# Kernel optimization log

Hardware: AMD Instinct MI355X
Metric: run time of the kernel (lower is better)

The kernel has to match this reference:

```python
import jax, jax.numpy as jnp
import numpy as np

B, D, H = 131072, 8, 128


def setup_inputs() -> dict:
    key = jax.random.key(0)
    ks = jax.random.split(key, 8)
    s1 = 1.0 / np.sqrt(D + 1)
    s2 = 1.0 / np.sqrt(H)
    return {
        "z": jax.random.normal(ks[0], (B, D), dtype=jnp.float32),
        "logp_z": jnp.zeros((B, 1), dtype=jnp.float32),
        "t": jax.random.uniform(ks[1], (1,), dtype=jnp.float32),
        "W1": jax.random.normal(ks[2], (D + 1, H), dtype=jnp.float32) * s1,
        "b1": jnp.zeros((H,), dtype=jnp.float32),
        "W2": jax.random.normal(ks[3], (H, H), dtype=jnp.float32) * s2,
        "b2": jnp.zeros((H,), dtype=jnp.float32),
        "W3": jax.random.normal(ks[4], (H, D), dtype=jnp.float32) * s2,
        "b3": jnp.zeros((D,), dtype=jnp.float32),
    }


def _net_single(z_i, t_scalar, W1, b1, W2, b2, W3, b3):
    # z_i: [D] -> dz/dt: [D]; FFJORD-style MLP on concat([z, t])
    x = jnp.concatenate([z_i, t_scalar[None]])  # [D+1]
    h = jnp.tanh(x @ W1 + b1)
    h = jnp.tanh(h @ W2 + b2)
    return h @ W3 + b3


def reference(z, logp_z, t, W1, b1, W2, b2, W3, b3):
    t_scalar = t.reshape(())

    def f_i(z_i):
        return _net_single(z_i, t_scalar, W1, b1, W2, b2, W3, b3)

    # dz/dt for every sample (batched forward)
    dz_dt = jax.vmap(f_i)(z)  # [B, D]
    # Exact Jacobian trace: fused forward-mode batched Jacobian (replaces the
    # original's D sequential autograd.grad reverse-mode calls)
    jac = jax.vmap(jax.jacfwd(f_i))(z)  # [B, D, D]
    trace = jnp.einsum("bii->b", jac)  # [B]
    dlogp_z_dt = -trace[:, None]  # [B, 1]
    return (dz_dt, dlogp_z_dt)
```

## Files before the change

### kernel.cpp

```cpp
#include <hip/hip_runtime.h>
#include <hip/hip_bf16.h>

#define BATCH 131072
#define PITCH_Q 40

typedef __bf16 bf16x8 __attribute__((ext_vector_type(8)));
typedef float floatx4 __attribute__((ext_vector_type(4)));

__device__ __forceinline__ float fast_tanh(float x) {
    float e = __expf(2.0f * x);
    return 1.0f - 2.0f * __builtin_amdgcn_rcpf(e + 1.0f);
}


__global__ void prep_kernel(const float* __restrict__ W1,
                            const float* __restrict__ W2,
                            const float* __restrict__ W3,
                            __bf16* __restrict__ ws) {
    int idx = blockIdx.x * 256 + threadIdx.x;
    if (idx < 16384) {
        int j = idx & 7, q = (idx >> 3) & 3, n = (idx >> 5) & 127, kb = idx >> 12;
        int k = kb * 32 + q * 8 + j;
        ws[idx] = (__bf16)W2[k * 128 + n];
        float c = 0.0f;
        #pragma unroll
        for (int d = 0; d < 8; ++d) c += W3[k * 8 + d] * W1[d * 128 + n];
        ws[16384 + idx] = (__bf16)(W2[n * 128 + k] * c);
    } else if (idx < 20480) {
        int t = idx - 16384;
        int j = t & 7, q = (t >> 3) & 3, n = t >> 5;
        int k = q * 8 + j;
        ws[32768 + t] = (k < 9) ? (__bf16)W1[k * 128 + n] : (__bf16)0.0f;
    } else if (idx < 22528) {
        int t = idx - 20480;
        int j = t & 7, q = (t >> 3) & 3, n = (t >> 5) & 15, kb = t >> 9;
        int k = kb * 32 + q * 8 + j;
        ws[36864 + t] = (n < 8) ? (__bf16)W3[k * 8 + n] : (__bf16)0.0f;
    }
}

__global__ __launch_bounds__(256, 2) void cnf_main(
        const float* __restrict__ z, const float* __restrict__ t_ptr,
        const float* __restrict__ b1g, const float* __restrict__ b2g,
        const float* __restrict__ b3g, const __bf16* __restrict__ ws,
        float* __restrict__ out) {
    __shared__ __bf16 sW2s[16384];
    __shared__ __bf16 sGTs[16384];
    __shared__ __align__(16) __bf16 tile[4][2][16 * PITCH_Q];

    const int tid = threadIdx.x;
    const int lane = tid & 63;
    const int w = tid >> 6;
    const int p = lane & 15;
    const int q = lane >> 4;
    const int sbase = blockIdx.x * 128 + w * 32;
    const float tval = t_ptr[0];

    bf16x8 ax0, ax1;
    #pragma unroll
    for (int j = 0; j < 8; ++j) { ax0[j] = (__bf16)0.0f; ax1[j] = (__bf16)0.0f; }
    if (q == 0) {
        const float4* zp0 = (const float4*)(z + (size_t)(sbase + p) * 8);
        const float4* zp1 = (const float4*)(z + (size_t)(sbase + 16 + p) * 8);
        const float4 a0 = zp0[0], a1 = zp0[1], c0 = zp1[0], c1 = zp1[1];
        ax0[0] = (__bf16)a0.x; ax0[1] = (__bf16)a0.y;
        ax0[2] = (__bf16)a0.z; ax0[3] = (__bf16)a0.w;
        ax0[4] = (__bf16)a1.x; ax0[5] = (__bf16)a1.y;
        ax0[6] = (__bf16)a1.z; ax0[7] = (__bf16)a1.w;
        ax1[0] = (__bf16)c0.x; ax1[1] = (__bf16)c0.y;
        ax1[2] = (__bf16)c0.z; ax1[3] = (__bf16)c0.w;
        ax1[4] = (__bf16)c1.x; ax1[5] = (__bf16)c1.y;
        ax1[6] = (__bf16)c1.z; ax1[7] = (__bf16)c1.w;
    } else if (q == 1) {
        ax0[0] = (__bf16)tval;
        ax1[0] = (__bf16)tval;
    }

    const bf16x8* W1g = (const bf16x8*)(ws + 32768);
    const bf16x8* W3g = (const bf16x8*)(ws + 36864);
    bf16x8 w1f[8];
    #pragma unroll
    for (int nt = 0; nt < 8; ++nt) w1f[nt] = W1g[(nt * 16 + p) * 4 + q];
    bf16x8 w3f[4];
    #pragma unroll
    for (int kb = 0; kb < 4; ++kb) w3f[kb] = W3g[(kb * 16 + p) * 4 + q];
    float b1f[8], b2f[8];
    #pragma unroll
    for (int nt = 0; nt < 8; ++nt) { b1f[nt] = b1g[nt * 16 + p]; b2f[nt] = b2g[nt * 16 + p]; }
    const float b3v = (p < 8) ? b3g[p] : 0.0f;

    {
        uint4* dst = (uint4*)sW2s;
        const uint4* src = (const uint4*)ws;
        #pragma unroll
        for (int i = 0; i < 8; ++i) dst[tid + i * 256] = src[tid + i * 256];
        uint4* dstg = (uint4*)sGTs;
        const uint4* srcg = (const uint4*)(ws + 16384);
        #pragma unroll
        for (int i = 0; i < 8; ++i) dstg[tid + i * 256] = srcg[tid + i * 256];
    }

    __bf16* Ta = tile[w][0];
    __bf16* Tb = tile[w][1];

    float a1c0[32], a1c1[32];
    bf16x8 ah0[4], ah1[4];
    #pragma unroll
    for (int c = 0; c < 4; ++c) {
        floatx4 aA[2], aB[2];
        #pragma unroll
        for (int lt = 0; lt < 2; ++lt) {
            floatx4 zz = {0.f, 0.f, 0.f, 0.f};
            aA[lt] = __builtin_amdgcn_mfma_f32_16x16x32_bf16(ax0, w1f[2 * c + lt], zz, 0, 0, 0);
            aB[lt] = __builtin_amdgcn_mfma_f32_16x16x32_bf16(ax1, w1f[2 * c + lt], zz, 0, 0, 0);
        }
        #pragma unroll
        for (int lt = 0; lt < 2; ++lt) {
            const int nt = 2 * c + lt;
            const float bn = b1f[nt];
            #pragma unroll
            for (int r = 0; r < 4; ++r) {
                const float h1a = fast_tanh(aA[lt][r] + bn);
                a1c0[nt * 4 + r] = __builtin_fmaf(-h1a, h1a, 1.0f);
                Ta[(q * 4 + r) * PITCH_Q + lt * 16 + p] = (__bf16)h1a;
                const float h1b = fast_tanh(aB[lt][r] + bn);
                a1c1[nt * 4 + r] = __builtin_fmaf(-h1b, h1b, 1.0f);
                Tb[(q * 4 + r) * PITCH_Q + lt * 16 + p] = (__bf16)h1b;
            }
        }
        ah0[c] = *(const bf16x8*)&Ta[p * PITCH_Q + q * 8];
        ah1[c] = *(const bf16x8*)&Tb[p * PITCH_Q + q * 8];
    }

    __syncthreads();
    const bf16x8* W2sv = (const bf16x8*)sW2s;
    const bf16x8* GTsv = (const bf16x8*)sGTs;

    bf16x8 ah2_0[4], ah2_1[4];
    #pragma unroll
    for (int c = 0; c < 4; ++c) {
        floatx4 aA[2] = {{0.f, 0.f, 0.f, 0.f}, {0.f, 0.f, 0.f, 0.f}};
        floatx4 aB[2] = {{0.f, 0.f, 0.f, 0.f}, {0.f, 0.f, 0.f, 0.f}};
        #pragma unroll
        for (int kb = 0; kb < 4; ++kb) {
            #pragma unroll
            for (int lt = 0; lt < 2; ++lt) {
                const int n = (2 * c + lt) * 16 + p;
                const bf16x8 wf = W2sv[(kb * 128 + n) * 4 + q];
                aA[lt] = __builtin_amdgcn_mfma_f32_16x16x32_bf16(ah0[kb], wf, aA[lt], 0, 0, 0);
                aB[lt] = __builtin_amdgcn_mfma_f32_16x16x32_bf16(ah1[kb], wf, aB[lt], 0, 0, 0);
            }
        }
        #pragma unroll
        for (int lt = 0; lt < 2; ++lt) {
            const int nt = 2 * c + lt;
            const float bn = b2f[nt];
            #pragma unroll
            for (int r = 0; r < 4; ++r) {
                const float h2a = fast_tanh(aA[lt][r] + bn);
                Ta[(q * 4 + r) * PITCH_Q + lt * 16 + p] = (__bf16)h2a;
                const float h2b = fast_tanh(aB[lt][r] + bn);
                Tb[(q * 4 + r) * PITCH_Q + lt * 16 + p] = (__bf16)h2b;
            }
        }
        ah2_0[c] = *(const bf16x8*)&Ta[p * PITCH_Q + q * 8];
        ah2_1[c] = *(const bf16x8*)&Tb[p * PITCH_Q + q * 8];
    }

    floatx4 d3A = {0.f, 0.f, 0.f, 0.f}, d3B = {0.f, 0.f, 0.f, 0.f};
    #pragma unroll
    for (int kb = 0; kb < 4; ++kb) {
        d3A = __builtin_amdgcn_mfma_f32_16x16x32_bf16(ah2_0[kb], w3f[kb], d3A, 0, 0, 0);
        d3B = __builtin_amdgcn_mfma_f32_16x16x32_bf16(ah2_1[kb], w3f[kb], d3B, 0, 0, 0);
    }
    if (p < 8) {
        #pragma unroll
        for (int r = 0; r < 4; ++r) {
            out[(size_t)(sbase + q * 4 + r) * 8 + p] = d3A[r] + b3v;
            out[(size_t)(sbase + 16 + q * 4 + r) * 8 + p] = d3B[r] + b3v;
        }
    }

    bf16x8 aa0[4], aa1[4];
    #pragma unroll
    for (int kb = 0; kb < 4; ++kb) {
        #pragma unroll
        for (int j = 0; j < 8; ++j) {
            const float fa = (float)ah2_0[kb][j];
            aa0[kb][j] = (__bf16)__builtin_fmaf(-fa, fa, 1.0f);
            const float fb = (float)ah2_1[kb][j];
            aa1[kb][j] = (__bf16)__builtin_fmaf(-fb, fb, 1.0f);
        }
    }

    float trA[4] = {0.f, 0.f, 0.f, 0.f}, trB[4] = {0.f, 0.f, 0.f, 0.f};
    #pragma unroll
    for (int nt = 0; nt < 8; ++nt) {
        const int n = nt * 16 + p;
        floatx4 uA = {0.f, 0.f, 0.f, 0.f}, uB = {0.f, 0.f, 0.f, 0.f};
        #pragma unroll
        for (int kb = 0; kb < 4; ++kb) {
            const bf16x8 gf = GTsv[(kb * 128 + n) * 4 + q];
            uA = __builtin_amdgcn_mfma_f32_16x16x32_bf16(aa0[kb], gf, uA, 0, 0, 0);
            uB = __builtin_amdgcn_mfma_f32_16x16x32_bf16(aa1[kb], gf, uB, 0, 0, 0);
        }
        #pragma unroll
        for (int r = 0; r < 4; ++r) {
            trA[r] = __builtin_fmaf(a1c0[nt * 4 + r], uA[r], trA[r]);
            trB[r] = __builtin_fmaf(a1c1[nt * 4 + r], uB[r], trB[r]);
        }
    }

    #pragma unroll
    for (int r = 0; r < 4; ++r) {
        float va = trA[r];
        va += __shfl_xor(va, 1, 64);
        va += __shfl_xor(va, 2, 64);
        va += __shfl_xor(va, 4, 64);
        va += __shfl_xor(va, 8, 64);
        trA[r] = va;
        float vb = trB[r];
        vb += __shfl_xor(vb, 1, 64);
        vb += __shfl_xor(vb, 2, 64);
        vb += __shfl_xor(vb, 4, 64);
        vb += __shfl_xor(vb, 8, 64);
        trB[r] = vb;
    }
    if (p == 0) {
        #pragma unroll
        for (int r = 0; r < 4; ++r) {
            out[(size_t)BATCH * 8 + sbase + q * 4 + r] = -trA[r];
            out[(size_t)BATCH * 8 + sbase + 16 + q * 4 + r] = -trB[r];
        }
    }
}

extern "C" void kernel_launch(void* const* d_in, const int* in_sizes, int n_in,
                              void* d_out, int out_size, void* d_ws, size_t ws_size,
                              hipStream_t stream) {
    const float* z  = (const float*)d_in[0];
    const float* t  = (const float*)d_in[2];
    const float* W1 = (const float*)d_in[3];
    const float* b1 = (const float*)d_in[4];
    const float* W2 = (const float*)d_in[5];
    const float* b2 = (const float*)d_in[6];
    const float* W3 = (const float*)d_in[7];
    const float* b3 = (const float*)d_in[8];
    __bf16* ws = (__bf16*)d_ws;
    float* out = (float*)d_out;

    prep_kernel<<<88, 256, 0, stream>>>(W1, W2, W3, ws);
    cnf_main<<<1024, 256, 0, stream>>>(z, t, b1, b2, b3, ws, out);
}
```

Baseline: 94.35 us.

## Transpose MFMA operand order, fold biases into accumulators and W1 padding

Swaps the A/B operands of every MFMA so outputs come out transposed (samples along lanes). Activations can then be written to the LDS tile as packed 4-element vectors, and outputs and traces stored with vector writes. The trace reduction becomes two cross-lane shuffles instead of four per row. b1 is folded into the padded K rows of W1 as a bf16 hi/lo split, b2 and b3 seed the accumulators, and the per-lane bias registers are dropped. The two per-wave tiles are merged into one wider tile. This cuts VALU work, LDS stores and register pressure, at the cost of slight precision changes in the bias handling.

```diff
diff --git a/kernel.cpp b/kernel.cpp
--- a/kernel.cpp
+++ b/kernel.cpp
@@ -2,8 +2,9 @@
 #include <hip/hip_bf16.h>
 
 #define BATCH 131072
-#define PITCH_Q 40
-
+#define PITCH_H 72
+
+typedef __bf16 bf16x4 __attribute__((ext_vector_type(4)));
 typedef __bf16 bf16x8 __attribute__((ext_vector_type(8)));
 typedef float floatx4 __attribute__((ext_vector_type(4)));
 
@@ -16,6 +17,7 @@
 __global__ void prep_kernel(const float* __restrict__ W1,
                             const float* __restrict__ W2,
                             const float* __restrict__ W3,
+                            const float* __restrict__ b1,
                             __bf16* __restrict__ ws) {
     int idx = blockIdx.x * 256 + threadIdx.x;
     if (idx < 16384) {
@@ -30,7 +32,14 @@
         int t = idx - 16384;
         int j = t & 7, q = (t >> 3) & 3, n = t >> 5;
         int k = q * 8 + j;
-        ws[32768 + t] = (k < 9) ? (__bf16)W1[k * 128 + n] : (__bf16)0.0f;
+        __bf16 v = (__bf16)0.0f;
+        if (k < 9) v = (__bf16)W1[k * 128 + n];
+        else if (k == 9) v = (__bf16)b1[n];
+        else if (k == 10) {
+            float hi = (float)(__bf16)b1[n];
+            v = (__bf16)(b1[n] - hi);
+        }
+        ws[32768 + t] = v;
     } else if (idx < 22528) {
         int t = idx - 20480;
         int j = t & 7, q = (t >> 3) & 3, n = (t >> 5) & 15, kb = t >> 9;
@@ -46,7 +55,8 @@
         float* __restrict__ out) {
     __shared__ __bf16 sW2s[16384];
     __shared__ __bf16 sGTs[16384];
-    __shared__ __align__(16) __bf16 tile[4][2][16 * PITCH_Q];
+    __shared__ float sb2f[128];
+    __shared__ __align__(16) __bf16 tile[4][16 * PITCH_H];
 
     const int tid = threadIdx.x;
     const int lane = tid & 63;
@@ -72,8 +82,8 @@
         ax1[4] = (__bf16)c1.x; ax1[5] = (__bf16)c1.y;
         ax1[6] = (__bf16)c1.z; ax1[7] = (__bf16)c1.w;
     } else if (q == 1) {
-        ax0[0] = (__bf16)tval;
-        ax1[0] = (__bf16)tval;
+        ax0[0] = (__bf16)tval; ax0[1] = (__bf16)1.0f; ax0[2] = (__bf16)1.0f;
+        ax1[0] = (__bf16)tval; ax1[1] = (__bf16)1.0f; ax1[2] = (__bf16)1.0f;
     }
 
     const bf16x8* W1g = (const bf16x8*)(ws + 32768);
@@ -84,10 +94,8 @@
     bf16x8 w3f[4];
     #pragma unroll
     for (int kb = 0; kb < 4; ++kb) w3f[kb] = W3g[(kb * 16 + p) * 4 + q];
-    float b1f[8], b2f[8];
-    #pragma unroll
-    for (int nt = 0; nt < 8; ++nt) { b1f[nt] = b1g[nt * 16 + p]; b2f[nt] = b2g[nt * 16 + p]; }
-    const float b3v = (p < 8) ? b3g[p] : 0.0f;
+    floatx4 b3f = {0.f, 0.f, 0.f, 0.f};
+    if (q < 2) b3f = *(const floatx4*)(b3g + q * 4);
 
     {
         uint4* dst = (uint4*)sW2s;
@@ -98,140 +106,137 @@
         const uint4* srcg = (const uint4*)(ws + 16384);
         #pragma unroll
         for (int i = 0; i < 8; ++i) dstg[tid + i * 256] = srcg[tid + i * 256];
-    }
-
-    __bf16* Ta = tile[w][0];
-    __bf16* Tb = tile[w][1];
+        if (tid < 128) sb2f[tid] = b2g[tid];
+    }
+
+    __bf16* T = tile[w];
 
     float a1c0[32], a1c1[32];
-    bf16x8 ah0[4], ah1[4];
-    #pragma unroll
-    for (int c = 0; c < 4; ++c) {
-        floatx4 aA[2], aB[2];
-        #pragma unroll
-        for (int lt = 0; lt < 2; ++lt) {
-            floatx4 zz = {0.f, 0.f, 0.f, 0.f};
-            aA[lt] = __builtin_amdgcn_mfma_f32_16x16x32_bf16(ax0, w1f[2 * c + lt], zz, 0, 0, 0);
-            aB[lt] = __builtin_amdgcn_mfma_f32_16x16x32_bf16(ax1, w1f[2 * c + lt], zz, 0, 0, 0);
-        }
-        #pragma unroll
-        for (int lt = 0; lt < 2; ++lt) {
-            const int nt = 2 * c + lt;
-            const float bn = b1f[nt];
+    bf16x8 aha[4], ahb[4];
+    #pragma unroll
+    for (int h = 0; h < 2; ++h) {
+        floatx4 accA[4], accB[4];
+        #pragma unroll
+        for (int lt = 0; lt < 4; ++lt) {
+            const floatx4 zz = {0.f, 0.f, 0.f, 0.f};
+            accA[lt] = __builtin_amdgcn_mfma_f32_16x16x32_bf16(w1f[4 * h + lt], ax0, zz, 0, 0, 0);
+            accB[lt] = __builtin_amdgcn_mfma_f32_16x16x32_bf16(w1f[4 * h + lt], ax1, zz, 0, 0, 0);
+        }
+        #pragma unroll
+        for (int lt = 0; lt < 4; ++lt) {
+            bf16x4 v;
             #pragma unroll
             for (int r = 0; r < 4; ++r) {
-                const float h1a = fast_tanh(aA[lt][r] + bn);
-                a1c0[nt * 4 + r] = __builtin_fmaf(-h1a, h1a, 1.0f);
-                Ta[(q * 4 + r) * PITCH_Q + lt * 16 + p] = (__bf16)h1a;
-                const float h1b = fast_tanh(aB[lt][r] + bn);
-                a1c1[nt * 4 + r] = __builtin_fmaf(-h1b, h1b, 1.0f);
-                Tb[(q * 4 + r) * PITCH_Q + lt * 16 + p] = (__bf16)h1b;
+                const float h1 = fast_tanh(accA[lt][r]);
+                a1c0[(4 * h + lt) * 4 + r] = __builtin_fmaf(-h1, h1, 1.0f);
+                v[r] = (__bf16)h1;
             }
-        }
-        ah0[c] = *(const bf16x8*)&Ta[p * PITCH_Q + q * 8];
-        ah1[c] = *(const bf16x8*)&Tb[p * PITCH_Q + q * 8];
+            *(bf16x4*)&T[p * PITCH_H + lt * 16 + q * 4] = v;
+        }
+        aha[2 * h]     = *(const bf16x8*)&T[p * PITCH_H + q * 8];
+        aha[2 * h + 1] = *(const bf16x8*)&T[p * PITCH_H + 32 + q * 8];
+        #pragma unroll
+        for (int lt = 0; lt < 4; ++lt) {
+            bf16x4 v;
+            #pragma unroll
+            for (int r = 0; r < 4; ++r) {
+                const float h1 = fast_tanh(accB[lt][r]);
+                a1c1[(4 * h + lt) * 4 + r] = __builtin_fmaf(-h1, h1, 1.0f);
+                v[r] = (__bf16)h1;
+            }
+            *(bf16x4*)&T[p * PITCH_H + lt * 16 + q * 4] = v;
+        }
+        ahb[2 * h]     = *(const bf16x8*)&T[p * PITCH_H + q * 8];
+        ahb[2 * h + 1] = *(const bf16x8*)&T[p * PITCH_H + 32 + q * 8];
     }
 
     __syncthreads();
     const bf16x8* W2sv = (const bf16x8*)sW2s;
     const bf16x8* GTsv = (const bf16x8*)sGTs;
 
-    bf16x8 ah2_0[4], ah2_1[4];
-    #pragma unroll
-    for (int c = 0; c < 4; ++c) {
-        floatx4 aA[2] = {{0.f, 0.f, 0.f, 0.f}, {0.f, 0.f, 0.f, 0.f}};
-        floatx4 aB[2] = {{0.f, 0.f, 0.f, 0.f}, {0.f, 0.f, 0.f, 0.f}};
+    bf16x8 ah2a[4], ah2b[4];
+    #pragma unroll
+    for (int h = 0; h < 2; ++h) {
+        floatx4 accA[4], accB[4];
+        #pragma unroll
+        for (int lt = 0; lt < 4; ++lt) {
+            const int nt = 4 * h + lt;
+            const floatx4 binit = *(const floatx4*)&sb2f[nt * 16 + q * 4];
+            floatx4 a = binit, b = binit;
+            #pragma unroll
+            for (int kb = 0; kb < 4; ++kb) {
+                const bf16x8 wf = W2sv[(kb * 128 + nt * 16 + p) * 4 + q];
+                a = __builtin_amdgcn_mfma_f32_16x16x32_bf16(wf, aha[kb], a, 0, 0, 0);
+                b = __builtin_amdgcn_mfma_f32_16x16x32_bf16(wf, ahb[kb], b, 0, 0, 0);
+            }
+            accA[lt] = a; accB[lt] = b;
+        }
+        #pragma unroll
+        for (int lt = 0; lt < 4; ++lt) {
+            bf16x4 v;
+            #pragma unroll
+            for (int r = 0; r < 4; ++r) v[r] = (__bf16)fast_tanh(accA[lt][r]);
+            *(bf16x4*)&T[p * PITCH_H + lt * 16 + q * 4] = v;
+        }
+        ah2a[2 * h]     = *(const bf16x8*)&T[p * PITCH_H + q * 8];
+        ah2a[2 * h + 1] = *(const bf16x8*)&T[p * PITCH_H + 32 + q * 8];
+        #pragma unroll
+        for (int lt = 0; lt < 4; ++lt) {
+            bf16x4 v;
+            #pragma unroll
+            for (int r = 0; r < 4; ++r) v[r] = (__bf16)fast_tanh(accB[lt][r]);
+            *(bf16x4*)&T[p * PITCH_H + lt * 16 + q * 4] = v;
+        }
+        ah2b[2 * h]     = *(const bf16x8*)&T[p * PITCH_H + q * 8];
+        ah2b[2 * h + 1] = *(const bf16x8*)&T[p * PITCH_H + 32 + q * 8];
+    }
+
+    floatx4 d3A = b3f, d3B = b3f;
+    #pragma unroll
+    for (int kb = 0; kb < 4; ++kb) {
+        d3A = __builtin_amdgcn_mfma_f32_16x16x32_bf16(w3f[kb], ah2a[kb], d3A, 0, 0, 0);
+        d3B = __builtin_amdgcn_mfma_f32_16x16x32_bf16(w3f[kb], ah2b[kb], d3B, 0, 0, 0);
+    }
+    if (q < 2) {
+        *(floatx4*)(out + (size_t)(sbase + p) * 8 + q * 4) = d3A;
+        *(floatx4*)(out + (size_t)(sbase + 16 + p) * 8 + q * 4) = d3B;
+    }
+
+    bf16x8 aaA[4], aaB[4];
+    #pragma unroll
+    for (int kb = 0; kb < 4; ++kb) {
+        #pragma unroll
+        for (int j = 0; j < 8; ++j) {
+            const float fa = (float)ah2a[kb][j];
+            aaA[kb][j] = (__bf16)__builtin_fmaf(-fa, fa, 1.0f);
+            const float fb = (float)ah2b[kb][j];
+            aaB[kb][j] = (__bf16)__builtin_fmaf(-fb, fb, 1.0f);
+        }
+    }
+
+    float trA = 0.f, trB = 0.f;
+    #pragma unroll
+    for (int nt = 0; nt < 8; ++nt) {
+        floatx4 uA = {0.f, 0.f, 0.f, 0.f}, uB = {0.f, 0.f, 0.f, 0.f};
         #pragma unroll
         for (int kb = 0; kb < 4; ++kb) {
-            #pragma unroll
-            for (int lt = 0; lt < 2; ++lt) {
-                const int n = (2 * c + lt) * 16 + p;
-                const bf16x8 wf = W2sv[(kb * 128 + n) * 4 + q];
-                aA[lt] = __builtin_amdgcn_mfma_f32_16x16x32_bf16(ah0[kb], wf, aA[lt], 0, 0, 0);
-                aB[lt] = __builtin_amdgcn_mfma_f32_16x16x32_bf16(ah1[kb], wf, aB[lt], 0, 0, 0);
-            }
-        }
-        #pragma unroll
-        for (int lt = 0; lt < 2; ++lt) {
-            const int nt = 2 * c + lt;
-            const float bn = b2f[nt];
-            #pragma unroll
-            for (int r = 0; r < 4; ++r) {
-                const float h2a = fast_tanh(aA[lt][r] + bn);
-                Ta[(q * 4 + r) * PITCH_Q + lt * 16 + p] = (__bf16)h2a;
-                const float h2b = fast_tanh(aB[lt][r] + bn);
-                Tb[(q * 4 + r) * PITCH_Q + lt * 16 + p] = (__bf16)h2b;
-            }
-        }
-        ah2_0[c] = *(const bf16x8*)&Ta[p * PITCH_Q + q * 8];
-        ah2_1[c] = *(const bf16x8*)&Tb[p * PITCH_Q + q * 8];
-    }
-
-    floatx4 d3A = {0.f, 0.f, 0.f, 0.f}, d3B = {0.f, 0.f, 0.f, 0.f};
-    #pragma unroll
-    for (int kb = 0; kb < 4; ++kb) {
-        d3A = __builtin_amdgcn_mfma_f32_16x16x32_bf16(ah2_0[kb], w3f[kb], d3A, 0, 0, 0);
-        d3B = __builtin_amdgcn_mfma_f32_16x16x32_bf16(ah2_1[kb], w3f[kb], d3B, 0, 0, 0);
-    }
-    if (p < 8) {
+            const bf16x8 gf = GTsv[(kb * 128 + nt * 16 + p) * 4 + q];
+            uA = __builtin_amdgcn_mfma_f32_16x16x32_bf16(gf, aaA[kb], uA, 0, 0, 0);
+            uB = __builtin_amdgcn_mfma_f32_16x16x32_bf16(gf, aaB[kb], uB, 0, 0, 0);
+        }
         #pragma unroll
         for (int r = 0; r < 4; ++r) {
-            out[(size_t)(sbase + q * 4 + r) * 8 + p] = d3A[r] + b3v;
-            out[(size_t)(sbase + 16 + q * 4 + r) * 8 + p] = d3B[r] + b3v;
-        }
-    }
-
-    bf16x8 aa0[4], aa1[4];
-    #pragma unroll
-    for (int kb = 0; kb < 4; ++kb) {
-        #pragma unroll
-        for (int j = 0; j < 8; ++j) {
-            const float fa = (float)ah2_0[kb][j];
-            aa0[kb][j] = (__bf16)__builtin_fmaf(-fa, fa, 1.0f);
-            const float fb = (float)ah2_1[kb][j];
-            aa1[kb][j] = (__bf16)__builtin_fmaf(-fb, fb, 1.0f);
-        }
-    }
-
-    float trA[4] = {0.f, 0.f, 0.f, 0.f}, trB[4] = {0.f, 0.f, 0.f, 0.f};
-    #pragma unroll
-    for (int nt = 0; nt < 8; ++nt) {
-        const int n = nt * 16 + p;
-        floatx4 uA = {0.f, 0.f, 0.f, 0.f}, uB = {0.f, 0.f, 0.f, 0.f};
-        #pragma unroll
-        for (int kb = 0; kb < 4; ++kb) {
-            const bf16x8 gf = GTsv[(kb * 128 + n) * 4 + q];
-            uA = __builtin_amdgcn_mfma_f32_16x16x32_bf16(aa0[kb], gf, uA, 0, 0, 0);
-            uB = __builtin_amdgcn_mfma_f32_16x16x32_bf16(aa1[kb], gf, uB, 0, 0, 0);
-        }
-        #pragma unroll
-        for (int r = 0; r < 4; ++r) {
-            trA[r] = __builtin_fmaf(a1c0[nt * 4 + r], uA[r], trA[r]);
-            trB[r] = __builtin_fmaf(a1c1[nt * 4 + r], uB[r], trB[r]);
-        }
-    }
-
-    #pragma unroll
-    for (int r = 0; r < 4; ++r) {
-        float va = trA[r];
-        va += __shfl_xor(va, 1, 64);
-        va += __shfl_xor(va, 2, 64);
-        va += __shfl_xor(va, 4, 64);
-        va += __shfl_xor(va, 8, 64);
-        trA[r] = va;
-        float vb = trB[r];
-        vb += __shfl_xor(vb, 1, 64);
-        vb += __shfl_xor(vb, 2, 64);
-        vb += __shfl_xor(vb, 4, 64);
-        vb += __shfl_xor(vb, 8, 64);
-        trB[r] = vb;
-    }
-    if (p == 0) {
-        #pragma unroll
-        for (int r = 0; r < 4; ++r) {
-            out[(size_t)BATCH * 8 + sbase + q * 4 + r] = -trA[r];
-            out[(size_t)BATCH * 8 + sbase + 16 + q * 4 + r] = -trB[r];
-        }
+            trA = __builtin_fmaf(a1c0[nt * 4 + r], uA[r], trA);
+            trB = __builtin_fmaf(a1c1[nt * 4 + r], uB[r], trB);
+        }
+    }
+    trA += __shfl_xor(trA, 16, 64);
+    trA += __shfl_xor(trA, 32, 64);
+    trB += __shfl_xor(trB, 16, 64);
+    trB += __shfl_xor(trB, 32, 64);
+    if (lane < 16) {
+        out[(size_t)BATCH * 8 + sbase + p] = -trA;
+        out[(size_t)BATCH * 8 + sbase + 16 + p] = -trB;
     }
 }
 
@@ -249,6 +254,6 @@
     __bf16* ws = (__bf16*)d_ws;
     float* out = (float*)d_out;
 
-    prep_kernel<<<88, 256, 0, stream>>>(W1, W2, W3, ws);
+    prep_kernel<<<88, 256, 0, stream>>>(W1, W2, W3, b1, ws);
     cnf_main<<<1024, 256, 0, stream>>>(z, t, b1, b2, b3, ws, out);
 }
```

New measurement: 89.95 us. 1.05x faster.
